# Performance work log

Measured on AMD Instinct MI355X. Metric: run time of the kernel, lower is better.

Reference implementation:

```python
import jax, jax.numpy as jnp
from jax import lax
import numpy as np
import math

# ---- static hyperparameters (from init_kwargs) ----
NUM_RAY = 64
NUM_RAY2 = NUM_RAY * NUM_RAY
NUM_SAMPLE = 64
STEP = 1.0 / (NUM_SAMPLE - 1)
RK = 3                       # RK4Range: neighbor cube side
K = 64                       # Num_RIGuassKernel per axis
PH = (192, 192, 192)         # PhantomSize (D, H, W)
THETA_X, THETA_Y, THETA_Z = 0.1, 0.05, 0.02
CENTER = (0.5, 0.5, 0.5)

# ---- constant neighbor offsets and kernel-center grids (Process_Parameter) ----
half = (RK - 1) // 2
_r = np.arange(-half, half + 1)
Xr_np, Yr_np, Zr_np = np.meshgrid(_r, _r, _r)
XR = jnp.asarray(Xr_np.flatten().reshape(1, RK ** 3), dtype=jnp.float32)
YR = jnp.asarray(Yr_np.flatten().reshape(1, RK ** 3), dtype=jnp.float32)
ZR = jnp.asarray(Zr_np.flatten().reshape(1, RK ** 3), dtype=jnp.float32)
_c = np.linspace(0, 1, K, dtype='float32')
Xc_np, Yc_np, Zc_np = np.meshgrid(_c, _c, _c)
XC = jnp.asarray(Xc_np.flatten())
YC = jnp.asarray(Yc_np.flatten())
ZC = jnp.asarray(Zc_np.flatten())

# ---- rotation matrices (Theta2TransMatrix) ----
def _build_transmats():
    def ry(t):
        c, s = math.cos(t), math.sin(t)
        return np.array([[1, 0, 0, 0], [0, c, -s, 0], [0, s, c, 0], [0, 0, 0, 1]], dtype=np.float64)
    def rx(t):
        c, s = math.cos(t), math.sin(t)
        return np.array([[c, 0, -s, 0], [0, 1, 0, 0], [s, 0, c, 0], [0, 0, 0, 1]], dtype=np.float64)
    def rz(t):
        c, s = math.cos(t), math.sin(t)
        return np.array([[c, -s, 0, 0], [s, c, 0, 0], [0, 0, 1, 0], [0, 0, 0, 1]], dtype=np.float64)
    RY, RY_ = ry(-THETA_Y), ry(THETA_Y)
    RX, RX_ = rx(THETA_X), rx(-THETA_X)
    RZ, RZ_ = rz(-THETA_Z), rz(THETA_Z)
    cx, cy, cz = CENTER
    S1 = np.eye(4); S1[3, :3] = [-cx, -cy, -cz]
    S2 = np.eye(4); S2[3, :3] = [cx, cy, cz]
    M_crd = S1 @ RZ @ RY @ RX @ S2
    M_drv = RX_ @ RY_ @ RZ_
    return jnp.asarray(M_crd, dtype=jnp.float32), jnp.asarray(M_drv, dtype=jnp.float32)

M_CRD, M_DRV = _build_transmats()


def _indexdist(x, y, z, RI):
    # x,y,z: [N]; RI: [K^3, 2] -> Gaussian-kernel interpolated n and spatial derivatives
    X, Y, Z = x[:, None], y[:, None], z[:, None]
    Xn = jnp.clip(jnp.round(X * K) + XR, 0.0, K - 1.0)
    Yn = jnp.clip(jnp.round(Y * K) + YR, 0.0, K - 1.0)
    Zn = jnp.clip(jnp.round(Z * K) + ZR, 0.0, K - 1.0)
    lin = (K * K * Yn + K * Xn + Zn).astype(jnp.int32)   # [N, RK^3]
    dx = XC[lin] - X
    dy = YC[lin] - Y
    dz = ZC[lin] - Z
    A = RI[lin, 0]
    sig = RI[lin, 1]
    inv_s2 = 1.0 / (sig * sig)
    ni = jnp.exp(-(dx * dx + dy * dy + dz * dz) * 0.5 * inv_s2) + 2e-7
    norm = jnp.sum(ni, axis=1)
    nu = ni * A
    nx = jnp.sum(nu * dx * inv_s2, axis=1)
    ny = jnp.sum(nu * dy * inv_s2, axis=1)
    nz = jnp.sum(nu * dz * inv_s2, axis=1)
    ndx = jnp.sum(ni * dx * inv_s2, axis=1)
    ndy = jnp.sum(ni * dy * inv_s2, axis=1)
    ndz = jnp.sum(ni * dz * inv_s2, axis=1)
    nu_s = jnp.sum(nu, axis=1)
    n = nu_s / norm
    inv_norm2 = 1.0 / (norm * norm)
    nx = (norm * nx - nu_s * ndx) * inv_norm2
    ny = (norm * ny - nu_s * ndy) * inv_norm2
    nz = (norm * nz - nu_s * ndz) * inv_norm2
    return n, nx, ny, nz


def _rayeq(z0, xy0, RI):
    ones = jnp.ones_like(z0)
    t = jnp.stack([xy0[:, 2], xy0[:, 0], z0, ones], axis=1) @ M_CRD
    n, dndx_, dndy_, dndz_ = _indexdist(t[:, 1], t[:, 0], t[:, 2], RI)
    d = jnp.stack([dndy_, dndx_, dndz_, ones], axis=1) @ M_DRV
    dndx, dndz, dndy = d[:, 1], d[:, 2], d[:, 0]
    dX1 = xy0[:, 1]
    dX2 = (dndx - dndz * dX1) * (1.0 + dX1 * dX1) / n
    dY1 = xy0[:, 3]
    dY2 = (dndy - dndz * dY1) * (1.0 + dY1 * dY1) / n
    return jnp.stack([dX1, dX2, dY1, dY2], axis=1)


def _ray_tracing(xyz0, RI):
    def step_fn(xyz, _):
        deriv = _rayeq(xyz[:, 4], xyz[:, 0:4], RI)
        xyzi = jnp.concatenate([xyz[:, 0:4] + deriv * STEP, (xyz[:, 4] + STEP)[:, None]], axis=1)
        return xyzi, xyzi
    _, rest = lax.scan(step_fn, xyz0, None, length=NUM_SAMPLE - 1)
    return jnp.concatenate([xyz0[None], rest], axis=0)   # [S, N, 5]


def _resize_axis_linear(a, axis, out_len):
    # align_corners=True 1D linear resize along `axis`
    in_len = a.shape[axis]
    pos = jnp.linspace(0.0, in_len - 1.0, out_len)
    i0 = jnp.clip(jnp.floor(pos).astype(jnp.int32), 0, in_len - 2)
    w = (pos - i0.astype(pos.dtype)).astype(a.dtype)
    a0 = jnp.take(a, i0, axis=axis)
    a1 = jnp.take(a, i0 + 1, axis=axis)
    shape = [1] * a.ndim
    shape[axis] = out_len
    w = w.reshape(shape)
    return a0 * (1.0 - w) + a1 * w


def _grid_sample_3d(vol, gx, gy, gz):
    # torch F.grid_sample trilinear, align_corners=True, padding_mode='zeros'
    D, H, W = vol.shape
    ix = (gx + 1.0) * 0.5 * (W - 1)
    iy = (gy + 1.0) * 0.5 * (H - 1)
    iz = (gz + 1.0) * 0.5 * (D - 1)
    x0 = jnp.floor(ix); y0 = jnp.floor(iy); z0 = jnp.floor(iz)
    fx = ix - x0; fy = iy - y0; fz = iz - z0
    out = jnp.zeros_like(ix)
    for dz in (0, 1):
        for dyy in (0, 1):
            for dxx in (0, 1):
                xi = x0 + dxx; yi = y0 + dyy; zi = z0 + dz
                wgt = (jnp.where(dxx == 1, fx, 1.0 - fx)
                       * jnp.where(dyy == 1, fy, 1.0 - fy)
                       * jnp.where(dz == 1, fz, 1.0 - fz))
                inb = ((xi >= 0) & (xi <= W - 1) & (yi >= 0) & (yi <= H - 1)
                       & (zi >= 0) & (zi <= D - 1))
                xc = jnp.clip(xi, 0, W - 1).astype(jnp.int32)
                yc = jnp.clip(yi, 0, H - 1).astype(jnp.int32)
                zc = jnp.clip(zi, 0, D - 1).astype(jnp.int32)
                out = out + jnp.where(inb, wgt * vol[zc, yc, xc], 0.0)
    return out


def setup_inputs() -> dict:
    key = jax.random.key(0)
    k1, k2, k3, k4, k5 = jax.random.split(key, 5)
    Phantom = jax.random.uniform(k1, (1, 1) + PH, dtype=jnp.float32)
    A = jax.random.uniform(k2, (K ** 3, 1), dtype=jnp.float32) * 0.9 + 0.1
    sig = jax.random.uniform(k3, (K ** 3, 1), dtype=jnp.float32) * 0.8 + 0.2
    RefractionIndex = jnp.concatenate([A, sig], axis=1)
    xy = jax.random.uniform(k4, (NUM_RAY2, 2), dtype=jnp.float32) * 0.8 + 0.1
    slopes = jax.random.normal(k5, (NUM_RAY2, 2), dtype=jnp.float32) * 0.05
    z0 = jnp.zeros((NUM_RAY2, 1), dtype=jnp.float32)
    # layout [x, dx/dz, y, dy/dz, z]
    RayInit = jnp.concatenate([xy[:, :1], slopes[:, :1], xy[:, 1:], slopes[:, 1:], z0], axis=1)
    return {"Phantom": Phantom, "RefractionIndex": RefractionIndex, "RayInit": RayInit}


def reference(Phantom, RefractionIndex, RayInit):
    RayInit = RayInit.reshape(NUM_RAY2, 5)
    RI = RefractionIndex.reshape(K ** 3, 2)
    paths = _ray_tracing(RayInit, RI)          # [S, N, 5]
    paths = paths * 2.0 - 1.0
    # paths -> [3, R, R, S] mesh of (x, y, z) coordinates
    mesh = jnp.stack([
        paths[:, :, 0].T.reshape(NUM_RAY, NUM_RAY, NUM_SAMPLE),
        paths[:, :, 2].T.reshape(NUM_RAY, NUM_RAY, NUM_SAMPLE),
        paths[:, :, 4].T.reshape(NUM_RAY, NUM_RAY, NUM_SAMPLE),
    ], axis=0)
    # trilinear resize (align_corners=True) to PhantomSize
    for ax, out_len in zip((1, 2, 3), PH):
        mesh = _resize_axis_linear(mesh, ax, out_len)   # [3, D, H, W]
    vol = Phantom.reshape(PH)
    out = _grid_sample_3d(vol, mesh[0], mesh[1], mesh[2])
    return out.reshape((1, 1) + PH)
```

## Files before the change

### kernel.cpp

```cpp
#include <hip/hip_runtime.h>
#include <math.h>

#define NRAY2 4096
#define NSAMP 64
#define PHD 192
#define PLANE (PHD*PHD)
constexpr float STEP = 1.0f / 63.0f;

struct Mats { float crd[16]; float drv[16]; };

static void mat_mul4(const double* A, const double* B, double* C) {
    for (int i = 0; i < 4; ++i)
        for (int j = 0; j < 4; ++j) {
            double s = 0.0;
            for (int k = 0; k < 4; ++k) s += A[i*4+k] * B[k*4+j];
            C[i*4+j] = s;
        }
}

static void build_mats(Mats& M) {
    const double tx = 0.1, ty = 0.05, tz = 0.02;
    const double cx = 0.5, cy = 0.5, cz = 0.5;
    auto ry = [](double t, double* m) {
        double c = cos(t), s = sin(t);
        double v[16] = {1,0,0,0, 0,c,-s,0, 0,s,c,0, 0,0,0,1};
        for (int i = 0; i < 16; ++i) m[i] = v[i];
    };
    auto rx = [](double t, double* m) {
        double c = cos(t), s = sin(t);
        double v[16] = {c,0,-s,0, 0,1,0,0, s,0,c,0, 0,0,0,1};
        for (int i = 0; i < 16; ++i) m[i] = v[i];
    };
    auto rz = [](double t, double* m) {
        double c = cos(t), s = sin(t);
        double v[16] = {c,-s,0,0, s,c,0,0, 0,0,1,0, 0,0,0,1};
        for (int i = 0; i < 16; ++i) m[i] = v[i];
    };
    double RY[16], RY_[16], RX[16], RX_[16], RZ[16], RZ_[16];
    ry(-ty, RY); ry(ty, RY_);
    rx(tx, RX);  rx(-tx, RX_);
    rz(-tz, RZ); rz(tz, RZ_);
    double S1[16] = {1,0,0,0, 0,1,0,0, 0,0,1,0, -cx,-cy,-cz,1};
    double S2[16] = {1,0,0,0, 0,1,0,0, 0,0,1,0,  cx, cy, cz,1};
    double t1[16], t2[16], t3[16], Mc[16], Md[16];
    mat_mul4(S1, RZ, t1);
    mat_mul4(t1, RY, t2);
    mat_mul4(t2, RX, t3);
    mat_mul4(t3, S2, Mc);
    mat_mul4(RX_, RY_, t1);
    mat_mul4(t1, RZ_, Md);
    for (int i = 0; i < 16; ++i) { M.crd[i] = (float)Mc[i]; M.drv[i] = (float)Md[i]; }
}

template<int CTRL>
__device__ __forceinline__ void dpp_level8(float* v) {
    int t[8];
    #pragma unroll
    for (int i = 0; i < 8; ++i)
        t[i] = __builtin_amdgcn_update_dpp(0, __float_as_int(v[i]), CTRL, 0xF, 0xF, true);
    #pragma unroll
    for (int i = 0; i < 8; ++i) v[i] += __int_as_float(t[i]);
}

__device__ __forceinline__ void red8(float* v) {
    dpp_level8<0x121>(v);
    dpp_level8<0x122>(v);
    dpp_level8<0x124>(v);
    dpp_level8<0x128>(v);
    int t[8];
    #pragma unroll
    for (int i = 0; i < 8; ++i)
        t[i] = __builtin_amdgcn_ds_swizzle(__float_as_int(v[i]), 0x401F);
    #pragma unroll
    for (int i = 0; i < 8; ++i) v[i] += __int_as_float(t[i]);
}

__global__ __launch_bounds__(256) void ray_trace_kernel(
    const float* __restrict__ RI,
    const float* __restrict__ RayInit,
    float* __restrict__ meshXT,
    float* __restrict__ meshYT,
    Mats M)
{
    const int tid = threadIdx.x;
    const int nb  = tid & 31;
    const int ray = blockIdx.x * 8 + (tid >> 5);
    const bool act = nb < 27;

    float xr = 0.f, yr = 0.f, zr = 0.f;
    if (act) {
        int a0 = nb / 9, a1 = (nb / 3) % 3, a2 = nb % 3;
        xr = (float)(a1 - 1);
        yr = (float)(a0 - 1);
        zr = (float)(a2 - 1);
    }

    float X  = RayInit[ray*5 + 0];
    float dX = RayInit[ray*5 + 1];
    float Y  = RayInit[ray*5 + 2];
    float dY = RayInit[ray*5 + 3];
    float z  = RayInit[ray*5 + 4];

    if (nb == 0) meshXT[ray] = X*2.0f - 1.0f;
    if (nb == 1) meshYT[ray] = Y*2.0f - 1.0f;

    auto prep = [&](float pX, float pY, float pz,
                    float& ox, float& oy, float& oz,
                    float& oXn, float& oYn, float& oZn) -> const float2* {
        float x  = pY*M.crd[1] + pX*M.crd[5] + pz*M.crd[9]  + M.crd[13];
        float y  = pY*M.crd[0] + pX*M.crd[4] + pz*M.crd[8]  + M.crd[12];
        float zz = pY*M.crd[2] + pX*M.crd[6] + pz*M.crd[10] + M.crd[14];
        float XnL = __builtin_amdgcn_fmed3f(rintf(x *64.0f) + xr, 0.0f, 63.0f);
        float YnL = __builtin_amdgcn_fmed3f(rintf(y *64.0f) + yr, 0.0f, 63.0f);
        float ZnL = __builtin_amdgcn_fmed3f(rintf(zz*64.0f) + zr, 0.0f, 63.0f);
        int lin = (int)(YnL*4096.0f + XnL*64.0f + ZnL);
        ox = x; oy = y; oz = zz; oXn = XnL; oYn = YnL; oZn = ZnL;
        return (const float2*)RI + lin;
    };

    float cx_, cy_, cz_, Xn, Yn, Zn;
    float2 ri = *prep(X, Y, z, cx_, cy_, cz_, Xn, Yn, Zn);

    for (int s = 1; s < NSAMP; ++s) {
        float nX = X + dX*STEP, nY = Y + dY*STEP, nz = z + STEP;
        float ncx, ncy, ncz, nXn, nYn, nZn;
        float2 ri_n = *prep(nX, nY, nz, ncx, ncy, ncz, nXn, nYn, nZn);

        float dx = Xn*(1.0f/63.0f) - cx_;
        float dy = Yn*(1.0f/63.0f) - cy_;
        float dz = Zn*(1.0f/63.0f) - cz_;
        float inv_s2 = __builtin_amdgcn_rcpf(ri.y * ri.y);
        float e = __expf(-(dx*dx + dy*dy + dz*dz) * 0.5f * inv_s2) + 2e-7f;
        if (!act) e = 0.0f;
        float gdx = dx*inv_s2, gdy = dy*inv_s2, gdz = dz*inv_s2;
        float nu  = e * ri.x;

        float v[8] = { e, nu, nu*gdx, nu*gdy, nu*gdz, e*gdx, e*gdy, e*gdz };
        red8(v);
        float ni  = v[0], nuA = v[1];
        float sx  = v[2], sy  = v[3], sz  = v[4];
        float sdx = v[5], sdy = v[6], sdz = v[7];

        float r   = __builtin_amdgcn_rcpf(ni);
        float rn  = ni * __builtin_amdgcn_rcpf(nuA);
        float in2 = r * r;
        float gx_ = (ni*sx - nuA*sdx) * in2;
        float gy_ = (ni*sy - nuA*sdy) * in2;
        float gz_ = (ni*sz - nuA*sdz) * in2;

        float dndx = gy_*M.drv[1] + gx_*M.drv[5] + gz_*M.drv[9]  + M.drv[13];
        float dndy = gy_*M.drv[0] + gx_*M.drv[4] + gz_*M.drv[8]  + M.drv[12];
        float dndz = gy_*M.drv[2] + gx_*M.drv[6] + gz_*M.drv[10] + M.drv[14];

        float dX2 = (dndx - dndz*dX) * (1.0f + dX*dX) * rn;
        float dY2 = (dndy - dndz*dY) * (1.0f + dY*dY) * rn;

        X = nX; Y = nY; z = nz;
        dX += dX2 * STEP;
        dY += dY2 * STEP;

        if (nb == 0) meshXT[s*NRAY2 + ray] = X*2.0f - 1.0f;
        if (nb == 1) meshYT[s*NRAY2 + ray] = Y*2.0f - 1.0f;

        cx_ = ncx; cy_ = ncy; cz_ = ncz;
        Xn = nXn; Yn = nYn; Zn = nZn;
        ri = ri_n;
    }
}

typedef _Float16 h16;
typedef _Float16 h16v4 __attribute__((ext_vector_type(4)));

__global__ __launch_bounds__(1024) void sample_kernel(
    const float* __restrict__ vol,
    const float* __restrict__ meshXT,
    const float* __restrict__ meshYT,
    h16*   __restrict__ outTh,
    float* __restrict__ outDirect,
    int transposed)
{
    __shared__ h16    plane_h[PLANE];
    __shared__ float2 slice[64*64];
    __shared__ float  wTab[PHD];
    __shared__ int    iTab[PHD];

    const int tid = threadIdx.x;
    const int blk = blockIdx.x;
    const int c = (blk >> 3) + 24 * (blk & 7);

    if (tid < PHD) {
        float p = tid * (63.0f / 191.0f);
        int i0 = min((int)p, 62);
        iTab[tid] = i0;
        wTab[tid] = p - (float)i0;
    }

    {
        const float4* src = (const float4*)(vol + c * PLANE);
        h16v4* dst = (h16v4*)plane_h;
        #pragma unroll
        for (int k = 0; k < (PLANE/4)/1024; ++k) {
            float4 v = src[tid + k*1024];
            h16v4 hv = {(h16)v.x, (h16)v.y, (h16)v.z, (h16)v.w};
            dst[tid + k*1024] = hv;
        }
    }

    float ps = c * (63.0f / 191.0f);
    int s0 = min((int)ps, 62);
    float wc = ps - (float)s0, wc0 = 1.0f - wc;
    {
        const float* x0 = meshXT + s0*NRAY2;
        const float* x1 = meshXT + (s0+1)*NRAY2;
        const float* y0 = meshYT + s0*NRAY2;
        const float* y1 = meshYT + (s0+1)*NRAY2;
        #pragma unroll
        for (int k = 0; k < 4096/1024; ++k) {
            int t = tid + k*1024;
            slice[t] = make_float2(x0[t]*wc0 + x1[t]*wc,
                                   y0[t]*wc0 + y1[t]*wc);
        }
    }
    __syncthreads();

    int a = tid / PHD, b = tid % PHD;
    #pragma unroll 2
    for (int k = 0; k < PLANE/1024; ++k) {
        int i0 = iTab[a]; float wa = wTab[a];
        int j0 = iTab[b]; float wb = wTab[b];

        float2 s00 = slice[i0*64 + j0];
        float2 s01 = slice[i0*64 + j0 + 1];
        float2 s10 = slice[(i0+1)*64 + j0];
        float2 s11 = slice[(i0+1)*64 + j0 + 1];

        float wb0 = 1.0f - wb, wa0 = 1.0f - wa;
        float gx = (s00.x*wb0 + s01.x*wb)*wa0 + (s10.x*wb0 + s11.x*wb)*wa;
        float gy = (s00.y*wb0 + s01.y*wb)*wa0 + (s10.y*wb0 + s11.y*wb)*wa;

        float ix = (gx + 1.0f) * 0.5f * 191.0f;
        float iy = (gy + 1.0f) * 0.5f * 191.0f;
        float x0f = floorf(ix); float fx = ix - x0f;
        float y0f = floorf(iy); float fy = iy - y0f;

        float acc = 0.0f;
        #pragma unroll
        for (int dyy = 0; dyy < 2; ++dyy) {
            #pragma unroll
            for (int dxx = 0; dxx < 2; ++dxx) {
                float xi = x0f + (float)dxx;
                float yi = y0f + (float)dyy;
                bool inb = (xi >= 0.0f) && (xi <= 191.0f) &&
                           (yi >= 0.0f) && (yi <= 191.0f);
                int xc = min(max((int)xi, 0), PHD - 1);
                int yc = min(max((int)yi, 0), PHD - 1);
                float w = (dxx ? fx : 1.0f - fx) * (dyy ? fy : 1.0f - fy);
                float val = (float)plane_h[yc*PHD + xc];
                acc += inb ? w * val : 0.0f;
            }
        }

        if (transposed) {
            outTh[c*PLANE + tid + k*1024] = (h16)acc;
        } else {
            outDirect[(a*PHD + b)*PHD + c] = acc;
        }

        a += 5; b += 64;
        if (b >= PHD) { b -= PHD; a += 1; }
    }
}

__global__ __launch_bounds__(256) void transpose_kernel(
    const h16* __restrict__ outTh, float* __restrict__ out)
{
    __shared__ h16 t[64][66];
    const int a  = blockIdx.z;
    const int b0 = blockIdx.x * 64;
    const int c0 = blockIdx.y * 64;
    const int tx = threadIdx.x & 63;
    const int ty = threadIdx.x >> 6;

    const h16* src = outTh + (size_t)(c0 + ty) * PLANE + a*PHD + b0 + tx;
    #pragma unroll
    for (int j = 0; j < 16; ++j)
        t[ty + 4*j][tx] = src[(size_t)(4*j) * PLANE];
    __syncthreads();

    float* dst = out + (size_t)a * PLANE + (size_t)(b0 + ty) * PHD + c0 + tx;
    #pragma unroll
    for (int j = 0; j < 16; ++j)
        dst[(size_t)(4*j) * PHD] = (float)t[tx][ty + 4*j];
}

extern "C" void kernel_launch(void* const* d_in, const int* in_sizes, int n_in,
                              void* d_out, int out_size, void* d_ws, size_t ws_size,
                              hipStream_t stream)
{
    const float* Phantom = (const float*)d_in[0];
    const float* RI      = (const float*)d_in[1];
    const float* RayInit = (const float*)d_in[2];
    float* out = (float*)d_out;

    float* meshXT = (float*)d_ws;
    float* meshYT = meshXT + NRAY2 * NSAMP;
    h16*   outTh  = (h16*)(meshYT + NRAY2 * NSAMP);

    const size_t need = (size_t)(2 * NRAY2 * NSAMP) * sizeof(float)
                      + (size_t)PHD * PLANE * sizeof(h16);
    const int use_transpose = (ws_size >= need) ? 1 : 0;

    Mats M;
    build_mats(M);

    ray_trace_kernel<<<NRAY2/8, 256, 0, stream>>>(RI, RayInit, meshXT, meshYT, M);

    if (use_transpose) {
        sample_kernel<<<PHD, 1024, 0, stream>>>(Phantom, meshXT, meshYT,
                                                outTh, nullptr, 1);
        transpose_kernel<<<dim3(3, 3, PHD), 256, 0, stream>>>(outTh, out);
    } else {
        sample_kernel<<<PHD, 1024, 0, stream>>>(Phantom, meshXT, meshYT,
                                                nullptr, out, 0);
    }
}
```

Baseline: 157.8 us.

## Pack 27 neighbor evaluations into 16 lanes per ray with two neighbors each

The ray tracer now assigns 16 lanes per ray instead of 32, with each lane evaluating two of the 27 neighbor kernels (lanes 0-10 take a second one). This drops the cross-half swizzle step from the reduction, so only DPP row reductions remain, and it halves the block count. It also cuts the lanes wasted on the 5 idle neighbor slots. In exchange each lane does two gathers and two exps per step, and there are fewer total waves for latency hiding. The sample kernel's unroll also goes from 2 to 4.

```diff
diff --git a/kernel.cpp b/kernel.cpp
--- a/kernel.cpp
+++ b/kernel.cpp
@@ -62,17 +62,11 @@
     for (int i = 0; i < 8; ++i) v[i] += __int_as_float(t[i]);
 }
 
-__device__ __forceinline__ void red8(float* v) {
+__device__ __forceinline__ void red8_16(float* v) {
     dpp_level8<0x121>(v);
     dpp_level8<0x122>(v);
     dpp_level8<0x124>(v);
     dpp_level8<0x128>(v);
-    int t[8];
-    #pragma unroll
-    for (int i = 0; i < 8; ++i)
-        t[i] = __builtin_amdgcn_ds_swizzle(__float_as_int(v[i]), 0x401F);
-    #pragma unroll
-    for (int i = 0; i < 8; ++i) v[i] += __int_as_float(t[i]);
 }
 
 __global__ __launch_bounds__(256) void ray_trace_kernel(
@@ -83,17 +77,13 @@
     Mats M)
 {
     const int tid = threadIdx.x;
-    const int nb  = tid & 31;
-    const int ray = blockIdx.x * 8 + (tid >> 5);
-    const bool act = nb < 27;
-
-    float xr = 0.f, yr = 0.f, zr = 0.f;
-    if (act) {
-        int a0 = nb / 9, a1 = (nb / 3) % 3, a2 = nb % 3;
-        xr = (float)(a1 - 1);
-        yr = (float)(a0 - 1);
-        zr = (float)(a2 - 1);
-    }
+    const int nb  = tid & 15;
+    const int ray = blockIdx.x * 16 + (tid >> 4);
+    const bool act2 = nb < 11;
+
+    const int n1 = nb, n2 = nb + 16;
+    const float xr1 = (float)((n1/3)%3 - 1), yr1 = (float)(n1/9 - 1), zr1 = (float)(n1%3 - 1);
+    const float xr2 = (float)((n2/3)%3 - 1), yr2 = (float)(n2/9 - 1), zr2 = (float)(n2%3 - 1);
 
     float X  = RayInit[ray*5 + 0];
     float dX = RayInit[ray*5 + 1];
@@ -106,37 +96,62 @@
 
     auto prep = [&](float pX, float pY, float pz,
                     float& ox, float& oy, float& oz,
-                    float& oXn, float& oYn, float& oZn) -> const float2* {
+                    float& X1, float& Y1, float& Z1,
+                    float& X2, float& Y2, float& Z2,
+                    float2& r1, float2& r2) {
         float x  = pY*M.crd[1] + pX*M.crd[5] + pz*M.crd[9]  + M.crd[13];
         float y  = pY*M.crd[0] + pX*M.crd[4] + pz*M.crd[8]  + M.crd[12];
         float zz = pY*M.crd[2] + pX*M.crd[6] + pz*M.crd[10] + M.crd[14];
-        float XnL = __builtin_amdgcn_fmed3f(rintf(x *64.0f) + xr, 0.0f, 63.0f);
-        float YnL = __builtin_amdgcn_fmed3f(rintf(y *64.0f) + yr, 0.0f, 63.0f);
-        float ZnL = __builtin_amdgcn_fmed3f(rintf(zz*64.0f) + zr, 0.0f, 63.0f);
-        int lin = (int)(YnL*4096.0f + XnL*64.0f + ZnL);
-        ox = x; oy = y; oz = zz; oXn = XnL; oYn = YnL; oZn = ZnL;
-        return (const float2*)RI + lin;
+        float rx_ = rintf(x*64.0f), ry_ = rintf(y*64.0f), rz_ = rintf(zz*64.0f);
+        X1 = __builtin_amdgcn_fmed3f(rx_ + xr1, 0.0f, 63.0f);
+        Y1 = __builtin_amdgcn_fmed3f(ry_ + yr1, 0.0f, 63.0f);
+        Z1 = __builtin_amdgcn_fmed3f(rz_ + zr1, 0.0f, 63.0f);
+        X2 = __builtin_amdgcn_fmed3f(rx_ + xr2, 0.0f, 63.0f);
+        Y2 = __builtin_amdgcn_fmed3f(ry_ + yr2, 0.0f, 63.0f);
+        Z2 = __builtin_amdgcn_fmed3f(rz_ + zr2, 0.0f, 63.0f);
+        int l1 = (int)(Y1*4096.0f + X1*64.0f + Z1);
+        int l2 = (int)(Y2*4096.0f + X2*64.0f + Z2);
+        r1 = ((const float2*)RI)[l1];
+        r2 = ((const float2*)RI)[l2];
+        ox = x; oy = y; oz = zz;
     };
 
-    float cx_, cy_, cz_, Xn, Yn, Zn;
-    float2 ri = *prep(X, Y, z, cx_, cy_, cz_, Xn, Yn, Zn);
+    float cx_, cy_, cz_, Xn1, Yn1, Zn1, Xn2, Yn2, Zn2;
+    float2 ri1, ri2;
+    prep(X, Y, z, cx_, cy_, cz_, Xn1, Yn1, Zn1, Xn2, Yn2, Zn2, ri1, ri2);
 
     for (int s = 1; s < NSAMP; ++s) {
         float nX = X + dX*STEP, nY = Y + dY*STEP, nz = z + STEP;
-        float ncx, ncy, ncz, nXn, nYn, nZn;
-        float2 ri_n = *prep(nX, nY, nz, ncx, ncy, ncz, nXn, nYn, nZn);
-
-        float dx = Xn*(1.0f/63.0f) - cx_;
-        float dy = Yn*(1.0f/63.0f) - cy_;
-        float dz = Zn*(1.0f/63.0f) - cz_;
-        float inv_s2 = __builtin_amdgcn_rcpf(ri.y * ri.y);
-        float e = __expf(-(dx*dx + dy*dy + dz*dz) * 0.5f * inv_s2) + 2e-7f;
-        if (!act) e = 0.0f;
-        float gdx = dx*inv_s2, gdy = dy*inv_s2, gdz = dz*inv_s2;
-        float nu  = e * ri.x;
-
-        float v[8] = { e, nu, nu*gdx, nu*gdy, nu*gdz, e*gdx, e*gdy, e*gdz };
-        red8(v);
+        float ncx, ncy, ncz, mX1, mY1, mZ1, mX2, mY2, mZ2;
+        float2 ri1n, ri2n;
+        prep(nX, nY, nz, ncx, ncy, ncz, mX1, mY1, mZ1, mX2, mY2, mZ2, ri1n, ri2n);
+
+        float dx1 = Xn1*(1.0f/63.0f) - cx_;
+        float dy1 = Yn1*(1.0f/63.0f) - cy_;
+        float dz1 = Zn1*(1.0f/63.0f) - cz_;
+        float is1 = __builtin_amdgcn_rcpf(ri1.y * ri1.y);
+        float e1  = __expf(-(dx1*dx1 + dy1*dy1 + dz1*dz1) * 0.5f * is1) + 2e-7f;
+        float g1x = dx1*is1, g1y = dy1*is1, g1z = dz1*is1;
+        float nu1 = e1 * ri1.x;
+
+        float dx2 = Xn2*(1.0f/63.0f) - cx_;
+        float dy2 = Yn2*(1.0f/63.0f) - cy_;
+        float dz2 = Zn2*(1.0f/63.0f) - cz_;
+        float is2 = __builtin_amdgcn_rcpf(ri2.y * ri2.y);
+        float e2  = __expf(-(dx2*dx2 + dy2*dy2 + dz2*dz2) * 0.5f * is2) + 2e-7f;
+        if (!act2) e2 = 0.0f;
+        float g2x = dx2*is2, g2y = dy2*is2, g2z = dz2*is2;
+        float nu2 = e2 * ri2.x;
+
+        float v[8] = { e1 + e2,
+                       nu1 + nu2,
+                       nu1*g1x + nu2*g2x,
+                       nu1*g1y + nu2*g2y,
+                       nu1*g1z + nu2*g2z,
+                       e1*g1x + e2*g2x,
+                       e1*g1y + e2*g2y,
+                       e1*g1z + e2*g2z };
+        red8_16(v);
         float ni  = v[0], nuA = v[1];
         float sx  = v[2], sy  = v[3], sz  = v[4];
         float sdx = v[5], sdy = v[6], sdz = v[7];
@@ -163,8 +178,9 @@
         if (nb == 1) meshYT[s*NRAY2 + ray] = Y*2.0f - 1.0f;
 
         cx_ = ncx; cy_ = ncy; cz_ = ncz;
-        Xn = nXn; Yn = nYn; Zn = nZn;
-        ri = ri_n;
+        Xn1 = mX1; Yn1 = mY1; Zn1 = mZ1;
+        Xn2 = mX2; Yn2 = mY2; Zn2 = mZ2;
+        ri1 = ri1n; ri2 = ri2n;
     }
 }
 
@@ -224,7 +240,7 @@
     __syncthreads();
 
     int a = tid / PHD, b = tid % PHD;
-    #pragma unroll 2
+    #pragma unroll 4
     for (int k = 0; k < PLANE/1024; ++k) {
         int i0 = iTab[a]; float wa = wTab[a];
         int j0 = iTab[b]; float wb = wTab[b];
@@ -313,7 +329,7 @@
     Mats M;
     build_mats(M);
 
-    ray_trace_kernel<<<NRAY2/8, 256, 0, stream>>>(RI, RayInit, meshXT, meshYT, M);
+    ray_trace_kernel<<<NRAY2/16, 256, 0, stream>>>(RI, RayInit, meshXT, meshYT, M);
 
     if (use_transpose) {
         sample_kernel<<<PHD, 1024, 0, stream>>>(Phantom, meshXT, meshYT,
```

After: 151.6 us. -3.9%, faster.
